# Kernel tuning notes

Hardware: AMD Instinct MI355X
Metric: run time of the kernel (lower is better)

## Reference

```python
import jax, jax.numpy as jnp
import numpy as np

D_IN = 1024
D_OUT = 1024
NUM_HEADS = 16
HEAD_DIM = D_OUT // NUM_HEADS


def setup_inputs() -> dict:
    key = jax.random.key(0)
    ks = jax.random.split(key, 6)
    B, S = 2, 2048
    scale = 1.0 / np.sqrt(D_IN)
    x = jax.random.normal(ks[0], (B, S, D_IN), dtype=jnp.float32)
    # Linear weights stored torch-style as [out_features, in_features]
    Wq = jax.random.normal(ks[1], (D_OUT, D_IN), dtype=jnp.float32) * scale
    Wk = jax.random.normal(ks[2], (D_OUT, D_IN), dtype=jnp.float32) * scale
    Wv = jax.random.normal(ks[3], (D_OUT, D_IN), dtype=jnp.float32) * scale
    Wo = jax.random.normal(ks[4], (D_OUT, D_IN), dtype=jnp.float32) * scale
    bo = jax.random.normal(ks[5], (D_OUT,), dtype=jnp.float32) * 0.01
    return {"x": x, "Wq": Wq, "Wk": Wk, "Wv": Wv, "Wo": Wo, "bo": bo}


def reference(x, Wq, Wk, Wv, Wo, bo):
    B, S, _ = x.shape
    H, hd = NUM_HEADS, HEAD_DIM
    # QKV projections (qkv_bias=False), split into heads: [B, H, S, hd]
    q = (x @ Wq.T).reshape(B, S, H, hd).transpose(0, 2, 1, 3)
    k = (x @ Wk.T).reshape(B, S, H, hd).transpose(0, 2, 1, 3)
    v = (x @ Wv.T).reshape(B, S, H, hd).transpose(0, 2, 1, 3)
    # scaled causal attention scores [B, H, S, S]
    scores = jnp.einsum("bhqd,bhkd->bhqk", q, k) / jnp.sqrt(jnp.float32(hd))
    causal = jnp.tril(jnp.ones((S, S), dtype=bool))
    scores = jnp.where(causal, scores, jnp.finfo(scores.dtype).min)
    attn = jax.nn.softmax(scores, axis=-1)  # dropout p=0.0 -> identity
    ctx = jnp.einsum("bhqk,bhkd->bhqd", attn, v)  # [B, H, S, hd]
    ctx = ctx.transpose(0, 2, 1, 3).reshape(B, S, H * hd)
    return ctx @ Wo.T + bo
```

## Files before the change

### kernel.cpp

```cpp
#include <hip/hip_runtime.h>
#include <hip/hip_bf16.h>

#define AS1 __attribute__((address_space(1)))
#define AS3 __attribute__((address_space(3)))

typedef __attribute__((ext_vector_type(4))) float floatx4;
typedef __attribute__((ext_vector_type(8))) short bf16x8;
typedef unsigned short u16;
typedef unsigned int u32;

__device__ __forceinline__ u16 f2b(float f) {
  u32 u = __builtin_bit_cast(u32, f);
  u += 0x7fffu + ((u >> 16) & 1u);
  return (u16)(u >> 16);
}
__device__ __forceinline__ u32 pk2(float lo, float hi) {
  __hip_bfloat162 h = __float22bfloat162_rn(float2{lo, hi});
  u32 u;
  __builtin_memcpy(&u, &h, 4);
  return u;
}
__device__ __forceinline__ bf16x8 cvt8(float4 a, float4 b) {
  uint4 u{pk2(a.x, a.y), pk2(a.z, a.w), pk2(b.x, b.y), pk2(b.z, b.w)};
  return __builtin_bit_cast(bf16x8, u);
}

__device__ __forceinline__ void gld16(const void* g, AS3 u32* l) {
  __builtin_amdgcn_global_load_lds((const AS1 u32*)(const AS1 void*)g, l, 16,
                                   0, 0);
}

#define QSCALE 0.18033688011112042f
#define QSHIFT 14.4269504088896f

__global__ __launch_bounds__(256) void cvt_all(
    const float* __restrict__ x, const float* __restrict__ wq,
    const float* __restrict__ wk, const float* __restrict__ wv,
    const float* __restrict__ wo, u16* __restrict__ xb, u16* __restrict__ wqb,
    u16* __restrict__ wkb, u16* __restrict__ wvb, u16* __restrict__ wob) {
  const int i = blockIdx.x * 256 + threadIdx.x;
  const float* src;
  u16* dst;
  int off;
  if (i < 524288) {
    src = x; dst = xb; off = i;
  } else {
    const int j = i - 524288;
    const int wsel = j >> 17;
    off = j & 131071;
    src = (wsel == 0) ? wq : (wsel == 1) ? wk : (wsel == 2) ? wv : wo;
    dst = (wsel == 0) ? wqb : (wsel == 1) ? wkb : (wsel == 2) ? wvb : wob;
  }
  const float4* p = (const float4*)(src + (size_t)off * 8);
  *(bf16x8*)(dst + (size_t)off * 8) = cvt8(p[0], p[1]);
}

__device__ __forceinline__ void gemm_bf16(const u16* __restrict__ A,
                                          const u16* __restrict__ B, short* sA,
                                          short* sB, floatx4 acc[4][4]) {
  const int tid = threadIdx.x;
  const int lane = tid & 63;
  const int w = tid >> 6;
  const int l15 = lane & 15, quad = lane >> 4;
  const int wm = w >> 1, wn = w & 1;

  const u16* ga = A + ((size_t)(w * 32 + (lane >> 2))) * 1024 + (lane & 3) * 8;
  const u16* gb = B + ((size_t)(w * 32 + (lane >> 2))) * 1024 + (lane & 3) * 8;
  AS3 u32* la = (AS3 u32*)(AS3 short*)sA + w * 512;
  AS3 u32* lb = (AS3 u32*)(AS3 short*)sB + w * 512;

  for (int kt = 0; kt < 32; ++kt) {
    __syncthreads();
    gld16(ga, la);
    gld16(ga + (size_t)16 * 1024, la + 256);
    gld16(gb, lb);
    gld16(gb + (size_t)16 * 1024, lb + 256);
    ga += 32;
    gb += 32;
    __syncthreads();

    bf16x8 af[4], bfr[4];
#pragma unroll
    for (int mc = 0; mc < 4; ++mc)
      af[mc] = *(const bf16x8*)&sA[(wm * 64 + mc * 16 + l15) * 32 + quad * 8];
#pragma unroll
    for (int nc = 0; nc < 4; ++nc)
      bfr[nc] = *(const bf16x8*)&sB[(wn * 64 + nc * 16 + l15) * 32 + quad * 8];
#pragma unroll
    for (int mc = 0; mc < 4; ++mc)
#pragma unroll
      for (int nc = 0; nc < 4; ++nc)
        acc[mc][nc] = __builtin_amdgcn_mfma_f32_16x16x32_bf16(
            af[mc], bfr[nc], acc[mc][nc], 0, 0, 0);
  }
}

__device__ __forceinline__ void qkv_epilogue(floatx4 acc[4][4], int m0, int nb,
                                             int sel, u16* __restrict__ Q,
                                             u16* __restrict__ K,
                                             u16* __restrict__ Vt) {
  const int tid = threadIdx.x;
  const int lane = tid & 63, w = tid >> 6;
  const int l15 = lane & 15, quad = lane >> 4;
  const int wm = w >> 1, wn = w & 1;
#pragma unroll
  for (int mc = 0; mc < 4; ++mc) {
#pragma unroll
    for (int nc = 0; nc < 4; ++nc) {
      const int nn = nb + wn * 64 + nc * 16 + l15;
      const int h = nn >> 6, d = nn & 63;
#pragma unroll
      for (int r = 0; r < 4; ++r) {
        const int m = m0 + wm * 64 + mc * 16 + quad * 4 + r;
        const int b = m >> 11, s = m & 2047;
        const int bh = b * 16 + h;
        float av = acc[mc][nc][r];
        if (sel == 0) av *= QSCALE;
        const u16 v = f2b(av);
        if (sel == 0)
          Q[((size_t)bh * 2048 + s) * 64 + d] = v;
        else if (sel == 1)
          K[((size_t)bh * 2048 + s) * 64 + d] = v;
        else
          Vt[((size_t)bh * 64 + d) * 2048 + s] = v;
      }
    }
  }
}

__global__ __launch_bounds__(256) void qkv_gemm_b(
    const u16* __restrict__ xb, const u16* __restrict__ Wqb,
    const u16* __restrict__ Wkb, const u16* __restrict__ Wvb,
    u16* __restrict__ Q, u16* __restrict__ K, u16* __restrict__ Vt) {
  __shared__ __align__(16) short smem[2 * 128 * 32];
  const int m0 = blockIdx.x * 128;
  const int by = blockIdx.y;
  const int sel = by >> 3;
  const int nb = (by & 7) * 128;
  const u16* W = (sel == 0) ? Wqb : (sel == 1) ? Wkb : Wvb;

  floatx4 acc[4][4];
#pragma unroll
  for (int i = 0; i < 4; i++)
#pragma unroll
    for (int j = 0; j < 4; j++) acc[i][j] = (floatx4)0.0f;
  gemm_bf16(xb + (size_t)m0 * 1024, W + (size_t)nb * 1024, smem,
            smem + 128 * 32, acc);
  qkv_epilogue(acc, m0, nb, sel, Q, K, Vt);
}

__global__ __launch_bounds__(256) void out_gemm_b(const u16* __restrict__ ctx,
                                                  const u16* __restrict__ Wob,
                                                  const float* __restrict__ bo,
                                                  float* __restrict__ out) {
  __shared__ __align__(16) short smem[2 * 128 * 32];
  const int tid = threadIdx.x;
  const int lane = tid & 63, w = tid >> 6;
  const int l15 = lane & 15, quad = lane >> 4;
  const int wm = w >> 1, wn = w & 1;
  const int m0 = blockIdx.x * 128;
  const int n0 = blockIdx.y * 128;

  floatx4 acc[4][4];
#pragma unroll
  for (int i = 0; i < 4; i++)
#pragma unroll
    for (int j = 0; j < 4; j++) acc[i][j] = (floatx4)0.0f;
  gemm_bf16(ctx + (size_t)m0 * 1024, Wob + (size_t)n0 * 1024, smem,
            smem + 128 * 32, acc);

#pragma unroll
  for (int mc = 0; mc < 4; ++mc)
#pragma unroll
    for (int nc = 0; nc < 4; ++nc) {
      const int n = n0 + wn * 64 + nc * 16 + l15;
      const float bias = bo[n];
#pragma unroll
      for (int r = 0; r < 4; ++r) {
        const int m = m0 + wm * 64 + mc * 16 + quad * 4 + r;
        out[(size_t)m * 1024 + n] = acc[mc][nc][r] + bias;
      }
    }
}

template <bool F32A>
__device__ __forceinline__ void gemm128(const void* __restrict__ A,
                                        const float* __restrict__ B, short* sA,
                                        short* sB, floatx4 acc[4][4]) {
  const int tid = threadIdx.x;
  const int lane = tid & 63;
  const int w = tid >> 6;
  const int l15 = lane & 15, quad = lane >> 4;
  const int wm = w >> 1, wn = w & 1;
  const int srow = tid >> 1;
  const int scb = (tid & 1) * 16;

  float4 pa[4], pb[4];
  int4 pa16[2];
  if constexpr (F32A) {
    const float* ap = (const float*)A + (size_t)srow * 1024 + scb;
    pa[0] = ((const float4*)ap)[0]; pa[1] = ((const float4*)ap)[1];
    pa[2] = ((const float4*)ap)[2]; pa[3] = ((const float4*)ap)[3];
  } else {
    const u16* ap = (const u16*)A + (size_t)srow * 1024 + scb;
    pa16[0] = ((const int4*)ap)[0]; pa16[1] = ((const int4*)ap)[1];
  }
  {
    const float* bp = B + (size_t)srow * 1024 + scb;
    pb[0] = ((const float4*)bp)[0]; pb[1] = ((const float4*)bp)[1];
    pb[2] = ((const float4*)bp)[2]; pb[3] = ((const float4*)bp)[3];
  }

  for (int kt = 0; kt < 32; ++kt) {
    __syncthreads();
    if constexpr (F32A) {
      *(bf16x8*)&sA[srow * 40 + scb] = cvt8(pa[0], pa[1]);
      *(bf16x8*)&sA[srow * 40 + scb + 8] = cvt8(pa[2], pa[3]);
    } else {
      *(int4*)&sA[srow * 40 + scb] = pa16[0];
      *(int4*)&sA[srow * 40 + scb + 8] = pa16[1];
    }
    *(bf16x8*)&sB[srow * 40 + scb] = cvt8(pb[0], pb[1]);
    *(bf16x8*)&sB[srow * 40 + scb + 8] = cvt8(pb[2], pb[3]);
    __syncthreads();

    if (kt < 31) {
      const int k0 = (kt + 1) * 32;
      if constexpr (F32A) {
        const float* ap = (const float*)A + (size_t)srow * 1024 + k0 + scb;
        pa[0] = ((const float4*)ap)[0]; pa[1] = ((const float4*)ap)[1];
        pa[2] = ((const float4*)ap)[2]; pa[3] = ((const float4*)ap)[3];
      } else {
        const u16* ap = (const u16*)A + (size_t)srow * 1024 + k0 + scb;
        pa16[0] = ((const int4*)ap)[0]; pa16[1] = ((const int4*)ap)[1];
      }
      const float* bp = B + (size_t)srow * 1024 + k0 + scb;
      pb[0] = ((const float4*)bp)[0]; pb[1] = ((const float4*)bp)[1];
      pb[2] = ((const float4*)bp)[2]; pb[3] = ((const float4*)bp)[3];
    }

    bf16x8 af[4], bfr[4];
#pragma unroll
    for (int mc = 0; mc < 4; ++mc)
      af[mc] = *(const bf16x8*)&sA[(wm * 64 + mc * 16 + l15) * 40 + quad * 8];
#pragma unroll
    for (int nc = 0; nc < 4; ++nc)
      bfr[nc] = *(const bf16x8*)&sB[(wn * 64 + nc * 16 + l15) * 40 + quad * 8];
#pragma unroll
    for (int mc = 0; mc < 4; ++mc)
#pragma unroll
      for (int nc = 0; nc < 4; ++nc)
        acc[mc][nc] = __builtin_amdgcn_mfma_f32_16x16x32_bf16(
            af[mc], bfr[nc], acc[mc][nc], 0, 0, 0);
  }
}

__global__ __launch_bounds__(256) void qkv_gemm_f(
    const float* __restrict__ x, const float* __restrict__ Wq,
    const float* __restrict__ Wk, const float* __restrict__ Wv,
    u16* __restrict__ Q, u16* __restrict__ K, u16* __restrict__ Vt) {
  __shared__ __align__(16) short smem[2 * 128 * 40];
  const int m0 = blockIdx.x * 128;
  const int by = blockIdx.y;
  const int sel = by >> 3;
  const int nb = (by & 7) * 128;
  const float* W = (sel == 0) ? Wq : (sel == 1) ? Wk : Wv;

  floatx4 acc[4][4];
#pragma unroll
  for (int i = 0; i < 4; i++)
#pragma unroll
    for (int j = 0; j < 4; j++) acc[i][j] = (floatx4)0.0f;
  gemm128<true>((const void*)(x + (size_t)m0 * 1024), W + (size_t)nb * 1024,
                smem, smem + 128 * 40, acc);
  qkv_epilogue(acc, m0, nb, sel, Q, K, Vt);
}

__global__ __launch_bounds__(256) void out_gemm_f(const u16* __restrict__ ctx,
                                                  const float* __restrict__ Wo,
                                                  const float* __restrict__ bo,
                                                  float* __restrict__ out) {
  __shared__ __align__(16) short smem[2 * 128 * 40];
  const int tid = threadIdx.x;
  const int lane = tid & 63, w = tid >> 6;
  const int l15 = lane & 15, quad = lane >> 4;
  const int wm = w >> 1, wn = w & 1;
  const int m0 = blockIdx.x * 128;
  const int n0 = blockIdx.y * 128;

  floatx4 acc[4][4];
#pragma unroll
  for (int i = 0; i < 4; i++)
#pragma unroll
    for (int j = 0; j < 4; j++) acc[i][j] = (floatx4)0.0f;
  gemm128<false>((const void*)(ctx + (size_t)m0 * 1024),
                 Wo + (size_t)n0 * 1024, smem, smem + 128 * 40, acc);

#pragma unroll
  for (int mc = 0; mc < 4; ++mc)
#pragma unroll
    for (int nc = 0; nc < 4; ++nc) {
      const int n = n0 + wn * 64 + nc * 16 + l15;
      const float bias = bo[n];
#pragma unroll
      for (int r = 0; r < 4; ++r) {
        const int m = m0 + wm * 64 + mc * 16 + quad * 4 + r;
        out[(size_t)m * 1024 + n] = acc[mc][nc][r] + bias;
      }
    }
}

__global__ __launch_bounds__(512, 2) void attn_kernel(
    const u16* __restrict__ Q, const u16* __restrict__ K,
    const u16* __restrict__ Vt, u16* __restrict__ ctx) {
  const int bid = blockIdx.x;
  const int pr = bid >> 5;
  const int bh = bid & 31;
  const int tid = threadIdx.x;
  const int w = tid >> 6;
  const int lane = tid & 63;
  const int l15 = lane & 15;
  const int quad = lane >> 4;

  __shared__ __align__(16) u16 sK[128 * 72];
  __shared__ __align__(16) u16 sV[64 * 136];

  const int kr = tid >> 2, kc = (tid & 3) * 16;
  const int vd = tid >> 3, vc = (tid & 7) * 16;
  const int b = bh >> 4, h = bh & 15;

  int4 pk[2], pv[2];
#pragma unroll
  for (int i = 0; i < 2; ++i) {
    pk[i] = *(const int4*)(K + ((size_t)bh * 2048 + kr) * 64 + kc + i * 8);
    pv[i] = *(const int4*)(Vt + ((size_t)bh * 64 + vd) * 2048 + vc + i * 8);
  }

  for (int half = 0; half < 2; ++half) {
    const int c = half ? pr : (15 - pr);
    const int wrow = c * 128 + w * 16;
    const int jbmax = c;

    bf16x8 aQ0, aQ1;
    {
      const u16* qp = Q + ((size_t)bh * 2048 + wrow + l15) * 64 + quad * 8;
      aQ0 = *(const bf16x8*)(qp);
      aQ1 = *(const bf16x8*)(qp + 32);
    }

    floatx4 accOT[4];
#pragma unroll
    for (int i = 0; i < 4; ++i) accOT[i] = (floatx4)0.0f;
    floatx4 lsv = (floatx4)0.0f;

    for (int jb = 0; jb <= jbmax; ++jb) {
      __syncthreads();
      *(int4*)&sK[kr * 72 + kc] = pk[0];
      *(int4*)&sK[kr * 72 + kc + 8] = pk[1];
      *(int4*)&sV[vd * 136 + vc] = pv[0];
      *(int4*)&sV[vd * 136 + vc + 8] = pv[1];
      __syncthreads();

      const int jn = (jb < jbmax) ? (jb + 1) * 128 : (half == 0 ? 0 : -1);
      if (jn >= 0) {
#pragma unroll
        for (int i = 0; i < 2; ++i) {
          pk[i] = *(const int4*)(K + ((size_t)bh * 2048 + jn + kr) * 64 + kc +
                                 i * 8);
          pv[i] = *(const int4*)(Vt + ((size_t)bh * 64 + vd) * 2048 + jn + vc +
                                 i * 8);
        }
      }

      const int jbase = jb * 128;
#pragma unroll
      for (int kp = 0; kp < 4; ++kp) {
        const int kbase = jbase + kp * 32;
        if (kbase > wrow + 15) break;

        const u16* kr0 = &sK[(kp * 32 + l15) * 72 + quad * 8];
        bf16x8 ak00 = *(const bf16x8*)(kr0);
        bf16x8 ak01 = *(const bf16x8*)(kr0 + 32);
        floatx4 st0 = (floatx4)0.0f;
        st0 = __builtin_amdgcn_mfma_f32_16x16x32_bf16(ak00, aQ0, st0, 0, 0, 0);
        st0 = __builtin_amdgcn_mfma_f32_16x16x32_bf16(ak01, aQ1, st0, 0, 0, 0);

        const bool have1 = (kbase + 16 <= wrow + 15);
        floatx4 st1 = (floatx4)0.0f;
        if (have1) {
          const u16* kr1 = kr0 + 16 * 72;
          bf16x8 ak10 = *(const bf16x8*)(kr1);
          bf16x8 ak11 = *(const bf16x8*)(kr1 + 32);
          st1 =
              __builtin_amdgcn_mfma_f32_16x16x32_bf16(ak10, aQ0, st1, 0, 0, 0);
          st1 =
              __builtin_amdgcn_mfma_f32_16x16x32_bf16(ak11, aQ1, st1, 0, 0, 0);
        }

        float p0[4], p1[4];
        const bool m0 = (kbase + 15 > wrow);
#pragma unroll
        for (int r = 0; r < 4; ++r) {
          float t = st0[r] - QSHIFT;
          if (m0 && (kbase + quad * 4 + r > wrow + l15)) t = -1e30f;
          p0[r] = __builtin_amdgcn_exp2f(t);
        }
        if (have1) {
          const bool m1 = (kbase + 31 > wrow);
#pragma unroll
          for (int r = 0; r < 4; ++r) {
            float t = st1[r] - QSHIFT;
            if (m1 && (kbase + 16 + quad * 4 + r > wrow + l15)) t = -1e30f;
            p1[r] = __builtin_amdgcn_exp2f(t);
          }
        } else {
          p1[0] = p1[1] = p1[2] = p1[3] = 0.0f;
        }
#pragma unroll
        for (int r = 0; r < 4; ++r) lsv[r] += p0[r] + p1[r];

        uint4 pfu{pk2(p0[0], p0[1]), pk2(p0[2], p0[3]), pk2(p1[0], p1[1]),
                  pk2(p1[2], p1[3])};
        const bf16x8 pf8 = __builtin_bit_cast(bf16x8, pfu);

#pragma unroll
        for (int dt = 0; dt < 4; ++dt) {
          const u16* vp = &sV[(dt * 16 + l15) * 136 + kp * 32 + quad * 4];
          uint2 v0 = *(const uint2*)(vp);
          uint2 v1 = *(const uint2*)(vp + 16);
          uint4 avu{v0.x, v0.y, v1.x, v1.y};
          bf16x8 av8 = __builtin_bit_cast(bf16x8, avu);
          accOT[dt] = __builtin_amdgcn_mfma_f32_16x16x32_bf16(av8, pf8,
                                                              accOT[dt], 0, 0,
                                                              0);
        }
      }
    }

    float lsum = (lsv[0] + lsv[1]) + (lsv[2] + lsv[3]);
    lsum += __shfl_xor(lsum, 16, 64);
    lsum += __shfl_xor(lsum, 32, 64);

    __syncthreads();
    const float inv = 1.0f / lsum;
    u16* tw = &sK[(w * 16) * 72];
#pragma unroll
    for (int dt = 0; dt < 4; ++dt) {
      uint2 o2{pk2(accOT[dt][0] * inv, accOT[dt][1] * inv),
               pk2(accOT[dt][2] * inv, accOT[dt][3] * inv)};
      *(uint2*)&tw[l15 * 72 + dt * 16 + quad * 4] = o2;
    }
    bf16x8 o0 = *(const bf16x8*)&tw[l15 * 72 + quad * 16];
    bf16x8 o1 = *(const bf16x8*)&tw[l15 * 72 + quad * 16 + 8];
    u16* cp = ctx + ((size_t)(b * 2048 + wrow + l15)) * 1024 + h * 64 +
              quad * 16;
    *(bf16x8*)cp = o0;
    *(bf16x8*)(cp + 8) = o1;
  }
}

extern "C" void kernel_launch(void* const* d_in, const int* in_sizes, int n_in,
                              void* d_out, int out_size, void* d_ws,
                              size_t ws_size, hipStream_t stream) {
  const float* x = (const float*)d_in[0];
  const float* Wq = (const float*)d_in[1];
  const float* Wk = (const float*)d_in[2];
  const float* Wv = (const float*)d_in[3];
  const float* Wo = (const float*)d_in[4];
  const float* bo = (const float*)d_in[5];
  float* out = (float*)d_out;

  u16* Q = (u16*)d_ws;
  u16* K = Q + (size_t)4096 * 1024;
  u16* Vt = K + (size_t)4096 * 1024;
  u16* ctx = Vt + (size_t)4096 * 1024;

  if (ws_size >= (size_t)40 * 1024 * 1024) {
    u16* xb = ctx;
    u16* Wqb = (u16*)d_ws + (size_t)16 * 1024 * 1024;
    u16* Wkb = Wqb + (size_t)1024 * 1024;
    u16* Wvb = Wkb + (size_t)1024 * 1024;
    u16* Wob = Wvb + (size_t)1024 * 1024;

    cvt_all<<<4096, 256, 0, stream>>>(x, Wq, Wk, Wv, Wo, xb, Wqb, Wkb, Wvb,
                                      Wob);
    qkv_gemm_b<<<dim3(32, 24), 256, 0, stream>>>(xb, Wqb, Wkb, Wvb, Q, K, Vt);
    attn_kernel<<<256, 512, 0, stream>>>(Q, K, Vt, ctx);
    out_gemm_b<<<dim3(32, 8), 256, 0, stream>>>(ctx, Wob, bo, out);
  } else {
    qkv_gemm_f<<<dim3(32, 24), 256, 0, stream>>>(x, Wq, Wk, Wv, Q, K, Vt);
    attn_kernel<<<256, 512, 0, stream>>>(Q, K, Vt, ctx);
    out_gemm_f<<<dim3(32, 8), 256, 0, stream>>>(ctx, Wo, bo, out);
  }
}
```

Before: 224.5 us.

## Double-buffer attention K/V tiles, split diagonal block path, retile output GEMM

The attention kernel now keeps two LDS buffers for K/V, so the next tile is stored into the spare buffer while the current one is consumed. This halves the barriers per iteration. Off-diagonal blocks take a mask-free path that software-pipelines the LDS fragment reads and raises wave priority around the MFMA groups. The output GEMM switches to 128x64 tiles with a direct global-to-LDS load loop, doubling the grid to 512 blocks for better CU coverage. In exchange, the doubled LDS use and extra registers may lower occupancy, and the new GEMM loop has no prefetch overlap.

```diff
diff --git a/kernel.cpp b/kernel.cpp
--- a/kernel.cpp
+++ b/kernel.cpp
@@ -153,31 +153,61 @@
                                                   const u16* __restrict__ Wob,
                                                   const float* __restrict__ bo,
                                                   float* __restrict__ out) {
-  __shared__ __align__(16) short smem[2 * 128 * 32];
+  __shared__ __align__(16) short smem[128 * 32 + 64 * 32];
   const int tid = threadIdx.x;
   const int lane = tid & 63, w = tid >> 6;
   const int l15 = lane & 15, quad = lane >> 4;
-  const int wm = w >> 1, wn = w & 1;
   const int m0 = blockIdx.x * 128;
-  const int n0 = blockIdx.y * 128;
-
-  floatx4 acc[4][4];
-#pragma unroll
-  for (int i = 0; i < 4; i++)
+  const int n0 = blockIdx.y * 64;
+  short* sA = smem;
+  short* sB = smem + 128 * 32;
+
+  const u16* ga = ctx + ((size_t)(m0 + w * 32 + (lane >> 2))) * 1024 +
+                  (lane & 3) * 8;
+  const u16* gb = Wob + ((size_t)(n0 + w * 16 + (lane >> 2))) * 1024 +
+                  (lane & 3) * 8;
+  AS3 u32* la = (AS3 u32*)(AS3 short*)sA + w * 512;
+  AS3 u32* lb = (AS3 u32*)(AS3 short*)sB + w * 256;
+
+  floatx4 acc[2][4];
+#pragma unroll
+  for (int i = 0; i < 2; i++)
 #pragma unroll
     for (int j = 0; j < 4; j++) acc[i][j] = (floatx4)0.0f;
-  gemm_bf16(ctx + (size_t)m0 * 1024, Wob + (size_t)n0 * 1024, smem,
-            smem + 128 * 32, acc);
-
-#pragma unroll
-  for (int mc = 0; mc < 4; ++mc)
+
+  for (int kt = 0; kt < 32; ++kt) {
+    __syncthreads();
+    gld16(ga, la);
+    gld16(ga + (size_t)16 * 1024, la + 256);
+    gld16(gb, lb);
+    ga += 32;
+    gb += 32;
+    __syncthreads();
+
+    bf16x8 af[2], bfr[4];
+#pragma unroll
+    for (int mc = 0; mc < 2; ++mc)
+      af[mc] = *(const bf16x8*)&sA[(w * 32 + mc * 16 + l15) * 32 + quad * 8];
+#pragma unroll
+    for (int nc = 0; nc < 4; ++nc)
+      bfr[nc] = *(const bf16x8*)&sB[(nc * 16 + l15) * 32 + quad * 8];
+#pragma unroll
+    for (int mc = 0; mc < 2; ++mc)
+#pragma unroll
+      for (int nc = 0; nc < 4; ++nc)
+        acc[mc][nc] = __builtin_amdgcn_mfma_f32_16x16x32_bf16(
+            af[mc], bfr[nc], acc[mc][nc], 0, 0, 0);
+  }
+
+#pragma unroll
+  for (int mc = 0; mc < 2; ++mc)
 #pragma unroll
     for (int nc = 0; nc < 4; ++nc) {
-      const int n = n0 + wn * 64 + nc * 16 + l15;
+      const int n = n0 + nc * 16 + l15;
       const float bias = bo[n];
 #pragma unroll
       for (int r = 0; r < 4; ++r) {
-        const int m = m0 + wm * 64 + mc * 16 + quad * 4 + r;
+        const int m = m0 + w * 32 + mc * 16 + quad * 4 + r;
         out[(size_t)m * 1024 + n] = acc[mc][nc][r] + bias;
       }
     }
@@ -322,24 +352,33 @@
   const int l15 = lane & 15;
   const int quad = lane >> 4;
 
-  __shared__ __align__(16) u16 sK[128 * 72];
-  __shared__ __align__(16) u16 sV[64 * 136];
+  constexpr int KE = 128 * 72;
+  constexpr int VE = 64 * 136;
+  constexpr int BUF = KE + VE;
+  __shared__ __align__(16) u16 lds[2 * BUF];
 
   const int kr = tid >> 2, kc = (tid & 3) * 16;
   const int vd = tid >> 3, vc = (tid & 7) * 16;
   const int b = bh >> 4, h = bh & 15;
 
+  const u16* Kg = K + (size_t)bh * 2048 * 64;
+  const u16* Vg = Vt + (size_t)bh * 64 * 2048;
+
   int4 pk[2], pv[2];
-#pragma unroll
-  for (int i = 0; i < 2; ++i) {
-    pk[i] = *(const int4*)(K + ((size_t)bh * 2048 + kr) * 64 + kc + i * 8);
-    pv[i] = *(const int4*)(Vt + ((size_t)bh * 64 + vd) * 2048 + vc + i * 8);
-  }
+  pk[0] = *(const int4*)(Kg + (size_t)kr * 64 + kc);
+  pk[1] = *(const int4*)(Kg + (size_t)kr * 64 + kc + 8);
+  pv[0] = *(const int4*)(Vg + (size_t)vd * 2048 + vc);
+  pv[1] = *(const int4*)(Vg + (size_t)vd * 2048 + vc + 8);
+  *(int4*)&lds[kr * 72 + kc] = pk[0];
+  *(int4*)&lds[kr * 72 + kc + 8] = pk[1];
+  *(int4*)&lds[KE + vd * 136 + vc] = pv[0];
+  *(int4*)&lds[KE + vd * 136 + vc + 8] = pv[1];
+  __syncthreads();
+  int cur = 0;
 
   for (int half = 0; half < 2; ++half) {
     const int c = half ? pr : (15 - pr);
     const int wrow = c * 128 + w * 16;
-    const int jbmax = c;
 
     bf16x8 aQ0, aQ1;
     {
@@ -353,97 +392,167 @@
     for (int i = 0; i < 4; ++i) accOT[i] = (floatx4)0.0f;
     floatx4 lsv = (floatx4)0.0f;
 
-    for (int jb = 0; jb <= jbmax; ++jb) {
-      __syncthreads();
-      *(int4*)&sK[kr * 72 + kc] = pk[0];
-      *(int4*)&sK[kr * 72 + kc + 8] = pk[1];
-      *(int4*)&sV[vd * 136 + vc] = pv[0];
-      *(int4*)&sV[vd * 136 + vc + 8] = pv[1];
-      __syncthreads();
-
-      const int jn = (jb < jbmax) ? (jb + 1) * 128 : (half == 0 ? 0 : -1);
+    for (int jb = 0; jb <= c; ++jb) {
+      const u16* sKb = lds + cur * BUF;
+      const u16* sVb = sKb + KE;
+
+      const int jn = (jb < c) ? (jb + 1) * 128 : (half == 0 ? 0 : -1);
       if (jn >= 0) {
-#pragma unroll
-        for (int i = 0; i < 2; ++i) {
-          pk[i] = *(const int4*)(K + ((size_t)bh * 2048 + jn + kr) * 64 + kc +
-                                 i * 8);
-          pv[i] = *(const int4*)(Vt + ((size_t)bh * 64 + vd) * 2048 + jn + vc +
-                                 i * 8);
+        pk[0] = *(const int4*)(Kg + (size_t)(jn + kr) * 64 + kc);
+        pk[1] = *(const int4*)(Kg + (size_t)(jn + kr) * 64 + kc + 8);
+        pv[0] = *(const int4*)(Vg + (size_t)vd * 2048 + jn + vc);
+        pv[1] = *(const int4*)(Vg + (size_t)vd * 2048 + jn + vc + 8);
+      }
+
+      if (jb < c) {
+        bf16x8 ka[2][4];
+        uint2 va[2][8];
+#pragma unroll
+        for (int u = 0; u < 4; ++u) {
+          const u16* kp0 = sKb + (0 * 32 + l15) * 72 + quad * 8;
+          ka[0][u] = *(const bf16x8*)(kp0 + (u >> 1) * (16 * 72) + (u & 1) * 32);
+        }
+#pragma unroll
+        for (int dt = 0; dt < 4; ++dt) {
+          const u16* vp = sVb + (dt * 16 + l15) * 136 + 0 * 32 + quad * 4;
+          va[0][2 * dt] = *(const uint2*)(vp);
+          va[0][2 * dt + 1] = *(const uint2*)(vp + 16);
+        }
+#pragma unroll
+        for (int kp = 0; kp < 4; ++kp) {
+          const int pc = kp & 1, pn = (kp + 1) & 1;
+          if (kp < 3) {
+            const u16* kp1 = sKb + ((kp + 1) * 32 + l15) * 72 + quad * 8;
+#pragma unroll
+            for (int u = 0; u < 4; ++u)
+              ka[pn][u] =
+                  *(const bf16x8*)(kp1 + (u >> 1) * (16 * 72) + (u & 1) * 32);
+#pragma unroll
+            for (int dt = 0; dt < 4; ++dt) {
+              const u16* vp =
+                  sVb + (dt * 16 + l15) * 136 + (kp + 1) * 32 + quad * 4;
+              va[pn][2 * dt] = *(const uint2*)(vp);
+              va[pn][2 * dt + 1] = *(const uint2*)(vp + 16);
+            }
+          }
+          floatx4 st0 = (floatx4)0.0f, st1 = (floatx4)0.0f;
+          __builtin_amdgcn_s_setprio(1);
+          st0 = __builtin_amdgcn_mfma_f32_16x16x32_bf16(ka[pc][0], aQ0, st0,
+                                                        0, 0, 0);
+          st1 = __builtin_amdgcn_mfma_f32_16x16x32_bf16(ka[pc][2], aQ0, st1,
+                                                        0, 0, 0);
+          st0 = __builtin_amdgcn_mfma_f32_16x16x32_bf16(ka[pc][1], aQ1, st0,
+                                                        0, 0, 0);
+          st1 = __builtin_amdgcn_mfma_f32_16x16x32_bf16(ka[pc][3], aQ1, st1,
+                                                        0, 0, 0);
+          __builtin_amdgcn_s_setprio(0);
+          float p0[4], p1[4];
+#pragma unroll
+          for (int r = 0; r < 4; ++r) {
+            p0[r] = __builtin_amdgcn_exp2f(st0[r] - QSHIFT);
+            p1[r] = __builtin_amdgcn_exp2f(st1[r] - QSHIFT);
+          }
+#pragma unroll
+          for (int r = 0; r < 4; ++r) lsv[r] += p0[r] + p1[r];
+          uint4 pfu{pk2(p0[0], p0[1]), pk2(p0[2], p0[3]), pk2(p1[0], p1[1]),
+                    pk2(p1[2], p1[3])};
+          const bf16x8 pf8 = __builtin_bit_cast(bf16x8, pfu);
+          __builtin_amdgcn_s_setprio(1);
+#pragma unroll
+          for (int dt = 0; dt < 4; ++dt) {
+            uint4 avu{va[pc][2 * dt].x, va[pc][2 * dt].y, va[pc][2 * dt + 1].x,
+                      va[pc][2 * dt + 1].y};
+            bf16x8 av8 = __builtin_bit_cast(bf16x8, avu);
+            accOT[dt] = __builtin_amdgcn_mfma_f32_16x16x32_bf16(
+                av8, pf8, accOT[dt], 0, 0, 0);
+          }
+          __builtin_amdgcn_s_setprio(0);
+        }
+      } else {
+        const int jbase = c * 128;
+#pragma unroll 2
+        for (int kp = 0; kp < 4; ++kp) {
+          const int kbase = jbase + kp * 32;
+          if (kbase > wrow + 15) break;
+
+          const u16* kr0 = sKb + (kp * 32 + l15) * 72 + quad * 8;
+          bf16x8 ak00 = *(const bf16x8*)(kr0);
+          bf16x8 ak01 = *(const bf16x8*)(kr0 + 32);
+          floatx4 st0 = (floatx4)0.0f;
+          st0 = __builtin_amdgcn_mfma_f32_16x16x32_bf16(ak00, aQ0, st0, 0, 0,
+                                                        0);
+          st0 = __builtin_amdgcn_mfma_f32_16x16x32_bf16(ak01, aQ1, st0, 0, 0,
+                                                        0);
+
+          const bool have1 = (kbase + 16 <= wrow + 15);
+          floatx4 st1 = (floatx4)0.0f;
+          if (have1) {
+            const u16* kr1 = kr0 + 16 * 72;
+            bf16x8 ak10 = *(const bf16x8*)(kr1);
+            bf16x8 ak11 = *(const bf16x8*)(kr1 + 32);
+            st1 = __builtin_amdgcn_mfma_f32_16x16x32_bf16(ak10, aQ0, st1, 0,
+                                                          0, 0);
+            st1 = __builtin_amdgcn_mfma_f32_16x16x32_bf16(ak11, aQ1, st1, 0,
+                                                          0, 0);
+          }
+
+          float p0[4], p1[4];
+          const bool m0b = (kbase + 15 > wrow);
+#pragma unroll
+          for (int r = 0; r < 4; ++r) {
+            float t = st0[r] - QSHIFT;
+            if (m0b && (kbase + quad * 4 + r > wrow + l15)) t = -1e30f;
+            p0[r] = __builtin_amdgcn_exp2f(t);
+          }
+          if (have1) {
+            const bool m1b = (kbase + 31 > wrow);
+#pragma unroll
+            for (int r = 0; r < 4; ++r) {
+              float t = st1[r] - QSHIFT;
+              if (m1b && (kbase + 16 + quad * 4 + r > wrow + l15)) t = -1e30f;
+              p1[r] = __builtin_amdgcn_exp2f(t);
+            }
+          } else {
+            p1[0] = p1[1] = p1[2] = p1[3] = 0.0f;
+          }
+#pragma unroll
+          for (int r = 0; r < 4; ++r) lsv[r] += p0[r] + p1[r];
+
+          uint4 pfu{pk2(p0[0], p0[1]), pk2(p0[2], p0[3]), pk2(p1[0], p1[1]),
+                    pk2(p1[2], p1[3])};
+          const bf16x8 pf8 = __builtin_bit_cast(bf16x8, pfu);
+
+#pragma unroll
+          for (int dt = 0; dt < 4; ++dt) {
+            const u16* vp = sVb + (dt * 16 + l15) * 136 + kp * 32 + quad * 4;
+            uint2 v0 = *(const uint2*)(vp);
+            uint2 v1 = *(const uint2*)(vp + 16);
+            uint4 avu{v0.x, v0.y, v1.x, v1.y};
+            bf16x8 av8 = __builtin_bit_cast(bf16x8, avu);
+            accOT[dt] = __builtin_amdgcn_mfma_f32_16x16x32_bf16(
+                av8, pf8, accOT[dt], 0, 0, 0);
+          }
         }
       }
 
-      const int jbase = jb * 128;
-#pragma unroll
-      for (int kp = 0; kp < 4; ++kp) {
-        const int kbase = jbase + kp * 32;
-        if (kbase > wrow + 15) break;
-
-        const u16* kr0 = &sK[(kp * 32 + l15) * 72 + quad * 8];
-        bf16x8 ak00 = *(const bf16x8*)(kr0);
-        bf16x8 ak01 = *(const bf16x8*)(kr0 + 32);
-        floatx4 st0 = (floatx4)0.0f;
-        st0 = __builtin_amdgcn_mfma_f32_16x16x32_bf16(ak00, aQ0, st0, 0, 0, 0);
-        st0 = __builtin_amdgcn_mfma_f32_16x16x32_bf16(ak01, aQ1, st0, 0, 0, 0);
-
-        const bool have1 = (kbase + 16 <= wrow + 15);
-        floatx4 st1 = (floatx4)0.0f;
-        if (have1) {
-          const u16* kr1 = kr0 + 16 * 72;
-          bf16x8 ak10 = *(const bf16x8*)(kr1);
-          bf16x8 ak11 = *(const bf16x8*)(kr1 + 32);
-          st1 =
-              __builtin_amdgcn_mfma_f32_16x16x32_bf16(ak10, aQ0, st1, 0, 0, 0);
-          st1 =
-              __builtin_amdgcn_mfma_f32_16x16x32_bf16(ak11, aQ1, st1, 0, 0, 0);
-        }
-
-        float p0[4], p1[4];
-        const bool m0 = (kbase + 15 > wrow);
-#pragma unroll
-        for (int r = 0; r < 4; ++r) {
-          float t = st0[r] - QSHIFT;
-          if (m0 && (kbase + quad * 4 + r > wrow + l15)) t = -1e30f;
-          p0[r] = __builtin_amdgcn_exp2f(t);
-        }
-        if (have1) {
-          const bool m1 = (kbase + 31 > wrow);
-#pragma unroll
-          for (int r = 0; r < 4; ++r) {
-            float t = st1[r] - QSHIFT;
-            if (m1 && (kbase + 16 + quad * 4 + r > wrow + l15)) t = -1e30f;
-            p1[r] = __builtin_amdgcn_exp2f(t);
-          }
-        } else {
-          p1[0] = p1[1] = p1[2] = p1[3] = 0.0f;
-        }
-#pragma unroll
-        for (int r = 0; r < 4; ++r) lsv[r] += p0[r] + p1[r];
-
-        uint4 pfu{pk2(p0[0], p0[1]), pk2(p0[2], p0[3]), pk2(p1[0], p1[1]),
-                  pk2(p1[2], p1[3])};
-        const bf16x8 pf8 = __builtin_bit_cast(bf16x8, pfu);
-
-#pragma unroll
-        for (int dt = 0; dt < 4; ++dt) {
-          const u16* vp = &sV[(dt * 16 + l15) * 136 + kp * 32 + quad * 4];
-          uint2 v0 = *(const uint2*)(vp);
-          uint2 v1 = *(const uint2*)(vp + 16);
-          uint4 avu{v0.x, v0.y, v1.x, v1.y};
-          bf16x8 av8 = __builtin_bit_cast(bf16x8, avu);
-          accOT[dt] = __builtin_amdgcn_mfma_f32_16x16x32_bf16(av8, pf8,
-                                                              accOT[dt], 0, 0,
-                                                              0);
-        }
+      if (jn >= 0) {
+        u16* dK = lds + (cur ^ 1) * BUF;
+        u16* dV = dK + KE;
+        *(int4*)&dK[kr * 72 + kc] = pk[0];
+        *(int4*)&dK[kr * 72 + kc + 8] = pk[1];
+        *(int4*)&dV[vd * 136 + vc] = pv[0];
+        *(int4*)&dV[vd * 136 + vc + 8] = pv[1];
       }
+      __syncthreads();
+      cur ^= 1;
     }
 
     float lsum = (lsv[0] + lsv[1]) + (lsv[2] + lsv[3]);
     lsum += __shfl_xor(lsum, 16, 64);
     lsum += __shfl_xor(lsum, 32, 64);
 
-    __syncthreads();
     const float inv = 1.0f / lsum;
-    u16* tw = &sK[(w * 16) * 72];
+    u16* tw = lds + (cur ^ 1) * BUF + (w * 16) * 72;
 #pragma unroll
     for (int dt = 0; dt < 4; ++dt) {
       uint2 o2{pk2(accOT[dt][0] * inv, accOT[dt][1] * inv),
@@ -456,6 +565,7 @@
               quad * 16;
     *(bf16x8*)cp = o0;
     *(bf16x8*)(cp + 8) = o1;
+    __syncthreads();
   }
 }
 
@@ -486,7 +596,7 @@
                                       Wob);
     qkv_gemm_b<<<dim3(32, 24), 256, 0, stream>>>(xb, Wqb, Wkb, Wvb, Q, K, Vt);
     attn_kernel<<<256, 512, 0, stream>>>(Q, K, Vt, ctx);
-    out_gemm_b<<<dim3(32, 8), 256, 0, stream>>>(ctx, Wob, bo, out);
+    out_gemm_b<<<dim3(32, 16), 256, 0, stream>>>(ctx, Wob, bo, out);
   } else {
     qkv_gemm_f<<<dim3(32, 24), 256, 0, stream>>>(x, Wq, Wk, Wv, Q, K, Vt);
     attn_kernel<<<256, 512, 0, stream>>>(Q, K, Vt, ctx);
```

Measured after the change: 196.3 us. 12.5% less time.
